# Optimization experiments

Measured on AMD Instinct MI355X. Metric: run time of the kernel, lower is better.

Reference implementation:

```python
import jax, jax.numpy as jnp
import numpy as np
import math

N_NODES = 100000
N_EDGES = 1600000
IN_C, HID_C, OUT_C = 512, 128, 64
N_LAYERS = 8
ALPHA = 0.1
THETA = 0.5


def setup_inputs() -> dict:
    key = jax.random.key(0)
    ks = jax.random.split(key, 6)
    x = jax.random.normal(ks[0], (N_NODES, IN_C), dtype=jnp.float32)
    edge_index = jax.random.randint(ks[1], (2, N_EDGES), 0, N_NODES, dtype=jnp.int32)
    edge_weight = jax.random.uniform(ks[2], (N_EDGES,), dtype=jnp.float32)
    # parameters (scaled for numerical sanity)
    W_enc = jax.random.normal(ks[3], (HID_C, IN_C), dtype=jnp.float32) * (1.0 / math.sqrt(IN_C))
    W_convs = jax.random.normal(ks[4], (N_LAYERS, HID_C, HID_C), dtype=jnp.float32) * (1.0 / math.sqrt(HID_C))
    W_dec = jax.random.normal(ks[5], (OUT_C, HID_C), dtype=jnp.float32) * (1.0 / math.sqrt(HID_C))
    return {"x": x, "edge_index": edge_index, "edge_weight": edge_weight,
            "W_enc": W_enc, "W_convs": W_convs, "W_dec": W_dec}


def reference(x, edge_index, edge_weight, W_enc, W_convs, W_dec):
    # eval mode: dropout is a no-op
    src, dst = edge_index[0], edge_index[1]
    h = x @ W_enc.T                      # [N, HID]
    x0 = h                               # initial residual
    for i in range(N_LAYERS):
        # sparse neighbor aggregation: agg[d] = sum_e w_e * h[src_e]
        msg = h[src] * edge_weight[:, None]                      # [E, HID]
        agg = jax.ops.segment_sum(msg, dst, num_segments=N_NODES)
        hh = (1.0 - ALPHA) * agg + ALPHA * x0                    # initial residual
        beta = math.log(THETA / (i + 1) + 1.0)                   # identity mapping weight
        h = jax.nn.relu((1.0 - beta) * hh + beta * (hh @ W_convs[i]))
    return h @ W_dec.T                   # [N, OUT]
```

## Files before the change

### kernel.cpp

```cpp
#include <hip/hip_runtime.h>
#include <math.h>

#define N_NODES 100000
#define N_EDGES 1600000
#define IN_C 512
#define HID_C 128
#define OUT_C 64
#define N_LAYERS 8

typedef short bf16x8 __attribute__((ext_vector_type(8)));
typedef float f32x4 __attribute__((ext_vector_type(4)));

static __device__ __forceinline__ ushort f2bf(float f) {
  uint u = __float_as_uint(f);
  u = (u + 0x7FFFu + ((u >> 16) & 1u)) >> 16;
  return (ushort)u;
}
static __device__ __forceinline__ float bflo(uint u) { return __uint_as_float(u << 16); }
static __device__ __forceinline__ float bfhi(uint u) { return __uint_as_float(u & 0xffff0000u); }

__global__ __launch_bounds__(256) void hist_kernel(const int* __restrict__ dst,
                                                   int* __restrict__ cnt) {
  int e = blockIdx.x * 256 + threadIdx.x;
  atomicAdd(&cnt[dst[e]], 1);
}

__global__ __launch_bounds__(256) void scan_block(const int* __restrict__ in,
                                                  int* __restrict__ out,
                                                  int* __restrict__ bsum, int n) {
  __shared__ int tsum[256];
  int t = threadIdx.x;
  int base = blockIdx.x * 1024 + t * 4;
  int v0 = (base + 0 < n) ? in[base + 0] : 0;
  int v1 = (base + 1 < n) ? in[base + 1] : 0;
  int v2 = (base + 2 < n) ? in[base + 2] : 0;
  int v3 = (base + 3 < n) ? in[base + 3] : 0;
  int s = v0 + v1 + v2 + v3;
  tsum[t] = s;
  __syncthreads();
  for (int off = 1; off < 256; off <<= 1) {
    int x = (t >= off) ? tsum[t - off] : 0;
    __syncthreads();
    tsum[t] += x;
    __syncthreads();
  }
  int excl = tsum[t] - s;
  int i0 = excl + v0, i1 = i0 + v1, i2 = i1 + v2, i3 = i2 + v3;
  if (base + 0 < n) out[base + 0] = i0;
  if (base + 1 < n) out[base + 1] = i1;
  if (base + 2 < n) out[base + 2] = i2;
  if (base + 3 < n) out[base + 3] = i3;
  if (t == 255 && bsum) bsum[blockIdx.x] = tsum[255];
}

__global__ __launch_bounds__(256) void finalize_rows(const int* __restrict__ incl,
                                                     const int* __restrict__ auxi,
                                                     int* __restrict__ row, int n) {
  int i = blockIdx.x * 256 + threadIdx.x;
  if (i < n) {
    int g = i >> 10;
    int off = g ? auxi[g - 1] : 0;
    row[i + 1] = incl[i] + off;
    if (i == 0) row[0] = 0;
  }
}

__global__ __launch_bounds__(128) void init_bincur(const int* __restrict__ row,
                                                   int* __restrict__ bincur) {
  int b = threadIdx.x;
  int n0 = b << 10;
  bincur[b] = row[n0 < N_NODES ? n0 : N_NODES];
}

__global__ __launch_bounds__(256) void bin_scatter(const int* __restrict__ src,
                                                   const int* __restrict__ dst,
                                                   const float* __restrict__ w,
                                                   int* __restrict__ bincur,
                                                   uint2* __restrict__ bb) {
  __shared__ uint2 ebuf[2048];
  __shared__ int hist[128];
  __shared__ int lstart[128];
  __shared__ int gbase[128];
  int tid = threadIdx.x;
  int base = blockIdx.x * 2048;
  int cnt = N_EDGES - base;
  if (cnt > 2048) cnt = 2048;
  if (tid < 128) hist[tid] = 0;
  __syncthreads();
  uint pay[8];
  int bn[8], rk[8], dfull[8];
#pragma unroll
  for (int i = 0; i < 8; i++) {
    int idx = tid + i * 256;
    if (idx < cnt) {
      int e = base + idx;
      int d = dst[e];
      uint fb = __float_as_uint(w[e]) + 0x8000u;
      pay[i] = ((fb >> 16) << 17) | (uint)src[e];
      dfull[i] = d;
      bn[i] = d >> 10;
      rk[i] = atomicAdd(&hist[bn[i]], 1);
    }
  }
  __syncthreads();
  if (tid == 0) {
    int acc = 0;
    for (int b = 0; b < 128; b++) { lstart[b] = acc; acc += hist[b]; }
  }
  __syncthreads();
  if (tid < 128 && hist[tid] > 0) gbase[tid] = atomicAdd(&bincur[tid], hist[tid]);
  __syncthreads();
#pragma unroll
  for (int i = 0; i < 8; i++) {
    int idx = tid + i * 256;
    if (idx < cnt) ebuf[lstart[bn[i]] + rk[i]] = make_uint2(pay[i], (uint)dfull[i]);
  }
  __syncthreads();
#pragma unroll
  for (int i = 0; i < 8; i++) {
    int j = tid + i * 256;
    if (j < cnt) {
      uint2 v = ebuf[j];
      int b = (int)(v.y >> 10);
      bb[gbase[b] + (j - lstart[b])] = v;
    }
  }
}

__global__ __launch_bounds__(256) void bin_place(const uint2* __restrict__ bb,
                                                 const int* __restrict__ row,
                                                 uint* __restrict__ epk) {
  __shared__ int lcur[1024];
  int b = blockIdx.x;
  int n0 = b << 10;
  int tid = threadIdx.x;
  for (int i = tid; i < 1024; i += 256) {
    int d = n0 + i;
    lcur[i] = (d < N_NODES) ? row[d] : 0;
  }
  __syncthreads();
  int hi = n0 + 1024;
  if (hi > N_NODES) hi = N_NODES;
  int beg = row[n0], end = row[hi];
  for (int j = beg + tid; j < end; j += 256) {
    uint2 v = bb[j];
    int p = atomicAdd(&lcur[v.y & 1023u], 1);
    epk[p] = v.x;
  }
}

__global__ __launch_bounds__(256) void cast_weights(const float* __restrict__ we,
                                                    const float* __restrict__ wc,
                                                    const float* __restrict__ wd,
                                                    ushort* __restrict__ web,
                                                    ushort* __restrict__ wcb,
                                                    ushort* __restrict__ wdb) {
  int i = blockIdx.x * 256 + threadIdx.x;
  if (i < 128 * 512) web[i] = f2bf(we[i]);
  if (i < 8 * 128 * 128) {
    int layer = i >> 14, rem = i & 16383, k = rem >> 7, j = rem & 127;
    wcb[(layer << 14) + (j << 7) + k] = f2bf(wc[i]);
  }
  if (i < 64 * 128) wdb[i] = f2bf(wd[i]);
}

__global__ __launch_bounds__(256) void enc_mfma(const float* __restrict__ x,
                                                const ushort* __restrict__ wb,
                                                ushort* __restrict__ h) {
  __shared__ ushort xs[32][136];
  __shared__ ushort ws[128][136];
  int tid = threadIdx.x;
  size_t row0 = (size_t)blockIdx.x * 32;
  int lane = tid & 63;
  int wv = tid >> 6;
  int m0 = (wv >> 1) * 16;
  int n0 = (wv & 1) * 64;
  int arow = m0 + (lane & 15);
  int akb = (lane >> 4) * 8;
  f32x4 acc[4] = {};
  for (int kc = 0; kc < 4; kc++) {
    int k0 = kc * 128;
    __syncthreads();
#pragma unroll
    for (int i = 0; i < 4; i++) {
      int u = tid + i * 256;
      int r = u >> 5, c4 = u & 31;
      float4 v = *(const float4*)(x + (row0 + r) * IN_C + k0 + c4 * 4);
      uint2 p;
      p.x = (uint)f2bf(v.x) | ((uint)f2bf(v.y) << 16);
      p.y = (uint)f2bf(v.z) | ((uint)f2bf(v.w) << 16);
      *(uint2*)&xs[r][c4 * 4] = p;
    }
#pragma unroll
    for (int i = 0; i < 8; i++) {
      int u = tid + i * 256;
      int c = u >> 4, o = u & 15;
      *(uint4*)&ws[c][o * 8] = *(const uint4*)(wb + (size_t)c * IN_C + k0 + o * 8);
    }
    __syncthreads();
#pragma unroll
    for (int ks = 0; ks < 4; ks++) {
      int kk = ks * 32 + akb;
      bf16x8 a = *(bf16x8*)&xs[arow][kk];
#pragma unroll
      for (int n = 0; n < 4; n++) {
        bf16x8 b = *(bf16x8*)&ws[n0 + n * 16 + (lane & 15)][kk];
        acc[n] = __builtin_amdgcn_mfma_f32_16x16x32_bf16(a, b, acc[n], 0, 0, 0);
      }
    }
  }
  int crow = m0 + (lane >> 4) * 4;
  int ccol = lane & 15;
#pragma unroll
  for (int n = 0; n < 4; n++)
#pragma unroll
    for (int r = 0; r < 4; r++)
      h[(row0 + crow + r) * HID_C + n0 + n * 16 + ccol] = f2bf(acc[n][r]);
}

__global__ __launch_bounds__(256) void agg_bf(const ushort* __restrict__ h,
                                              const ushort* __restrict__ x0,
                                              const int* __restrict__ row,
                                              const uint* __restrict__ epk,
                                              ushort* __restrict__ out) {
  int node = (blockIdx.x * 256 + threadIdx.x) >> 6;
  int lane = threadIdx.x & 63;
  int beg = row[node], end = row[node + 1];
  float a0 = 0.f, a1 = 0.f;
  const uint* hp = (const uint*)h + lane;
  for (int e = beg; e < end; e += 8) {
    uint p0 = (e + 0 < end) ? epk[e + 0] : 0u;
    uint p1 = (e + 1 < end) ? epk[e + 1] : 0u;
    uint p2 = (e + 2 < end) ? epk[e + 2] : 0u;
    uint p3 = (e + 3 < end) ? epk[e + 3] : 0u;
    uint p4 = (e + 4 < end) ? epk[e + 4] : 0u;
    uint p5 = (e + 5 < end) ? epk[e + 5] : 0u;
    uint p6 = (e + 6 < end) ? epk[e + 6] : 0u;
    uint p7 = (e + 7 < end) ? epk[e + 7] : 0u;
    uint h0 = hp[(size_t)(p0 & 0x1FFFFu) * 64];
    uint h1 = hp[(size_t)(p1 & 0x1FFFFu) * 64];
    uint h2 = hp[(size_t)(p2 & 0x1FFFFu) * 64];
    uint h3 = hp[(size_t)(p3 & 0x1FFFFu) * 64];
    uint h4 = hp[(size_t)(p4 & 0x1FFFFu) * 64];
    uint h5 = hp[(size_t)(p5 & 0x1FFFFu) * 64];
    uint h6 = hp[(size_t)(p6 & 0x1FFFFu) * 64];
    uint h7 = hp[(size_t)(p7 & 0x1FFFFu) * 64];
    float w0 = __uint_as_float((p0 >> 17) << 16);
    float w1 = __uint_as_float((p1 >> 17) << 16);
    float w2 = __uint_as_float((p2 >> 17) << 16);
    float w3 = __uint_as_float((p3 >> 17) << 16);
    float w4 = __uint_as_float((p4 >> 17) << 16);
    float w5 = __uint_as_float((p5 >> 17) << 16);
    float w6 = __uint_as_float((p6 >> 17) << 16);
    float w7 = __uint_as_float((p7 >> 17) << 16);
    a0 = fmaf(w0, bflo(h0), a0); a1 = fmaf(w0, bfhi(h0), a1);
    a0 = fmaf(w1, bflo(h1), a0); a1 = fmaf(w1, bfhi(h1), a1);
    a0 = fmaf(w2, bflo(h2), a0); a1 = fmaf(w2, bfhi(h2), a1);
    a0 = fmaf(w3, bflo(h3), a0); a1 = fmaf(w3, bfhi(h3), a1);
    a0 = fmaf(w4, bflo(h4), a0); a1 = fmaf(w4, bfhi(h4), a1);
    a0 = fmaf(w5, bflo(h5), a0); a1 = fmaf(w5, bfhi(h5), a1);
    a0 = fmaf(w6, bflo(h6), a0); a1 = fmaf(w6, bfhi(h6), a1);
    a0 = fmaf(w7, bflo(h7), a0); a1 = fmaf(w7, bfhi(h7), a1);
  }
  uint xv = ((const uint*)x0)[(size_t)node * 64 + lane];
  float o0 = 0.9f * a0 + 0.1f * bflo(xv);
  float o1 = 0.9f * a1 + 0.1f * bfhi(xv);
  ((uint*)out)[(size_t)node * 64 + lane] = (uint)f2bf(o0) | ((uint)f2bf(o1) << 16);
}

__global__ __launch_bounds__(256) void conv_mfma(ushort* __restrict__ hbuf,
                                                 const ushort* __restrict__ wb,
                                                 float onemb, float beta) {
  __shared__ ushort hs[64][136];
  __shared__ ushort ws[128][136];
  int tid = threadIdx.x;
  size_t row0 = (size_t)blockIdx.x * 64;
#pragma unroll
  for (int i = 0; i < 4; i++) {
    int u = tid + i * 256;
    int r = u >> 4, o = u & 15;
    if (row0 + r < N_NODES)
      *(uint4*)&hs[r][o * 8] = *(const uint4*)(hbuf + (row0 + r) * HID_C + o * 8);
  }
#pragma unroll
  for (int i = 0; i < 8; i++) {
    int u = tid + i * 256;
    int c = u >> 4, o = u & 15;
    *(uint4*)&ws[c][o * 8] = *(const uint4*)(wb + (size_t)c * HID_C + o * 8);
  }
  __syncthreads();
  int lane = tid & 63;
  int wv = tid >> 6;
  int m0 = wv * 16;
  int arow = m0 + (lane & 15), akb = (lane >> 4) * 8;
  f32x4 acc[8] = {};
#pragma unroll
  for (int ks = 0; ks < 4; ks++) {
    int kk = ks * 32 + akb;
    bf16x8 a = *(bf16x8*)&hs[arow][kk];
#pragma unroll
    for (int n = 0; n < 8; n++) {
      bf16x8 b = *(bf16x8*)&ws[n * 16 + (lane & 15)][kk];
      acc[n] = __builtin_amdgcn_mfma_f32_16x16x32_bf16(a, b, acc[n], 0, 0, 0);
    }
  }
  int crow = m0 + (lane >> 4) * 4, ccol = lane & 15;
#pragma unroll
  for (int n = 0; n < 8; n++)
#pragma unroll
    for (int r = 0; r < 4; r++) {
      if (row0 + crow + r < N_NODES) {
        float hv = bflo((uint)hs[crow + r][n * 16 + ccol]);
        float o = fmaxf(onemb * hv + beta * acc[n][r], 0.f);
        hbuf[(row0 + crow + r) * HID_C + n * 16 + ccol] = f2bf(o);
      }
    }
}

__global__ __launch_bounds__(256) void dec_mfma(const ushort* __restrict__ h,
                                                const ushort* __restrict__ wb,
                                                float* __restrict__ out) {
  __shared__ ushort hs[32][136];
  __shared__ ushort ws[64][136];
  int tid = threadIdx.x;
  size_t row0 = (size_t)blockIdx.x * 32;
  {
    int r = tid >> 3, o = tid & 7;
    *(uint4*)&hs[r][o * 16] = *(const uint4*)(h + (row0 + r) * HID_C + o * 16);
    *(uint4*)&hs[r][o * 16 + 8] = *(const uint4*)(h + (row0 + r) * HID_C + o * 16 + 8);
  }
#pragma unroll
  for (int i = 0; i < 4; i++) {
    int u = tid + i * 256;
    int c = u >> 4, o = u & 15;
    *(uint4*)&ws[c][o * 8] = *(const uint4*)(wb + (size_t)c * HID_C + o * 8);
  }
  __syncthreads();
  int lane = tid & 63, wv = tid >> 6;
  int m0 = (wv >> 1) * 16, n0 = (wv & 1) * 32;
  int arow = m0 + (lane & 15), akb = (lane >> 4) * 8;
  f32x4 acc[2] = {};
#pragma unroll
  for (int ks = 0; ks < 4; ks++) {
    int kk = ks * 32 + akb;
    bf16x8 a = *(bf16x8*)&hs[arow][kk];
#pragma unroll
    for (int n = 0; n < 2; n++) {
      bf16x8 b = *(bf16x8*)&ws[n0 + n * 16 + (lane & 15)][kk];
      acc[n] = __builtin_amdgcn_mfma_f32_16x16x32_bf16(a, b, acc[n], 0, 0, 0);
    }
  }
  int crow = m0 + (lane >> 4) * 4, ccol = lane & 15;
#pragma unroll
  for (int n = 0; n < 2; n++)
#pragma unroll
    for (int r = 0; r < 4; r++)
      out[(row0 + crow + r) * OUT_C + n0 + n * 16 + ccol] = acc[n][r];
}

extern "C" void kernel_launch(void* const* d_in, const int* in_sizes, int n_in,
                              void* d_out, int out_size, void* d_ws, size_t ws_size,
                              hipStream_t stream) {
  const float* x = (const float*)d_in[0];
  const int* ei = (const int*)d_in[1];
  const float* ew = (const float*)d_in[2];
  const float* Wenc = (const float*)d_in[3];
  const float* Wconvs = (const float*)d_in[4];
  const float* Wdec = (const float*)d_in[5];
  float* out = (float*)d_out;

  char* p = (char*)d_ws;
  ushort* H0 = (ushort*)p; p += (size_t)N_NODES * HID_C * 2;
  ushort* HA = (ushort*)p; p += (size_t)N_NODES * HID_C * 2;
  ushort* HB = (ushort*)p; p += (size_t)N_NODES * HID_C * 2;
  uint* EPK = (uint*)p;    p += (size_t)N_EDGES * 4;
  uint2* BB = (uint2*)p;   p += (size_t)N_EDGES * 8;
  ushort* WENC = (ushort*)p;  p += 128 * 512 * 2;
  ushort* WCONV = (ushort*)p; p += 8 * 128 * 128 * 2;
  ushort* WDEC = (ushort*)p;  p += 64 * 128 * 2;
  int* ROW = (int*)p;  p += (N_NODES + 1) * 4;
  int* CNT = (int*)p;  p += N_NODES * 4;
  int* INCL = (int*)p; p += N_NODES * 4;
  int* BINCUR = (int*)p; p += 128 * 4;
  int* AUX = (int*)p;  p += 128 * 4;
  int* AUXI = (int*)p;

  const int* src = ei;
  const int* dst = ei + N_EDGES;

  cast_weights<<<512, 256, 0, stream>>>(Wenc, Wconvs, Wdec, WENC, WCONV, WDEC);

  hipMemsetAsync(CNT, 0, N_NODES * sizeof(int), stream);
  hist_kernel<<<N_EDGES / 256, 256, 0, stream>>>(dst, CNT);
  scan_block<<<98, 256, 0, stream>>>(CNT, INCL, AUX, N_NODES);
  scan_block<<<1, 256, 0, stream>>>(AUX, AUXI, nullptr, 98);
  finalize_rows<<<391, 256, 0, stream>>>(INCL, AUXI, ROW, N_NODES);
  init_bincur<<<1, 128, 0, stream>>>(ROW, BINCUR);
  bin_scatter<<<(N_EDGES + 2047) / 2048, 256, 0, stream>>>(src, dst, ew, BINCUR, BB);
  bin_place<<<98, 256, 0, stream>>>(BB, ROW, EPK);

  enc_mfma<<<3125, 256, 0, stream>>>(x, WENC, H0);

  const ushort* cur = H0;
  ushort* bufs[2] = {HA, HB};
  for (int i = 0; i < N_LAYERS; i++) {
    ushort* nxt = bufs[i & 1];
    agg_bf<<<25000, 256, 0, stream>>>(cur, H0, ROW, EPK, nxt);
    float beta = logf(0.5f / (float)(i + 1) + 1.0f);
    conv_mfma<<<1563, 256, 0, stream>>>(nxt, WCONV + (size_t)i * HID_C * HID_C,
                                        1.0f - beta, beta);
    cur = nxt;
  }

  dec_mfma<<<3125, 256, 0, stream>>>(cur, WDEC, out);
}
```

Measured before the change: 847.7 us.

## Bin edges into fixed-stride buckets first, enlarge encoder tile, deepen gather unroll

```diff
diff --git a/kernel.cpp b/kernel.cpp
--- a/kernel.cpp
+++ b/kernel.cpp
@@ -7,6 +7,7 @@
 #define HID_C 128
 #define OUT_C 64
 #define N_LAYERS 8
+#define BINSTRIDE 18432
 
 typedef short bf16x8 __attribute__((ext_vector_type(8)));
 typedef float f32x4 __attribute__((ext_vector_type(4)));
@@ -19,10 +20,80 @@
 static __device__ __forceinline__ float bflo(uint u) { return __uint_as_float(u << 16); }
 static __device__ __forceinline__ float bfhi(uint u) { return __uint_as_float(u & 0xffff0000u); }
 
-__global__ __launch_bounds__(256) void hist_kernel(const int* __restrict__ dst,
-                                                   int* __restrict__ cnt) {
-  int e = blockIdx.x * 256 + threadIdx.x;
-  atomicAdd(&cnt[dst[e]], 1);
+__global__ __launch_bounds__(128) void init_bincur(int* __restrict__ bincur) {
+  bincur[threadIdx.x] = threadIdx.x * BINSTRIDE;
+}
+
+__global__ __launch_bounds__(256) void bin_scatter(const int* __restrict__ src,
+                                                   const int* __restrict__ dst,
+                                                   const float* __restrict__ w,
+                                                   int* __restrict__ bincur,
+                                                   uint2* __restrict__ bb) {
+  __shared__ uint2 ebuf[2048];
+  __shared__ int hist[128];
+  __shared__ int lstart[128];
+  __shared__ int gbase[128];
+  int tid = threadIdx.x;
+  int base = blockIdx.x * 2048;
+  int cnt = N_EDGES - base;
+  if (cnt > 2048) cnt = 2048;
+  if (tid < 128) hist[tid] = 0;
+  __syncthreads();
+  uint pay[8];
+  int bn[8], rk[8], dfull[8];
+#pragma unroll
+  for (int i = 0; i < 8; i++) {
+    int idx = tid + i * 256;
+    if (idx < cnt) {
+      int e = base + idx;
+      int d = dst[e];
+      uint fb = __float_as_uint(w[e]) + 0x8000u;
+      pay[i] = ((fb >> 16) << 17) | (uint)src[e];
+      dfull[i] = d;
+      bn[i] = d >> 10;
+      rk[i] = atomicAdd(&hist[bn[i]], 1);
+    }
+  }
+  __syncthreads();
+  if (tid == 0) {
+    int acc = 0;
+    for (int b = 0; b < 128; b++) { lstart[b] = acc; acc += hist[b]; }
+  }
+  __syncthreads();
+  if (tid < 128 && hist[tid] > 0) gbase[tid] = atomicAdd(&bincur[tid], hist[tid]);
+  __syncthreads();
+#pragma unroll
+  for (int i = 0; i < 8; i++) {
+    int idx = tid + i * 256;
+    if (idx < cnt) ebuf[lstart[bn[i]] + rk[i]] = make_uint2(pay[i], (uint)dfull[i]);
+  }
+  __syncthreads();
+#pragma unroll
+  for (int i = 0; i < 8; i++) {
+    int j = tid + i * 256;
+    if (j < cnt) {
+      uint2 v = ebuf[j];
+      int b = (int)(v.y >> 10);
+      bb[gbase[b] + (j - lstart[b])] = v;
+    }
+  }
+}
+
+__global__ __launch_bounds__(256) void bin_count(const uint2* __restrict__ bb,
+                                                 const int* __restrict__ bincur,
+                                                 int* __restrict__ cnt) {
+  __shared__ int lc[1024];
+  int b = blockIdx.x;
+  int tid = threadIdx.x;
+  for (int i = tid; i < 1024; i += 256) lc[i] = 0;
+  __syncthreads();
+  int beg = b * BINSTRIDE, end = bincur[b];
+  for (int j = beg + tid; j < end; j += 256)
+    atomicAdd(&lc[bb[j].y & 1023u], 1);
+  __syncthreads();
+  int n0 = b << 10;
+  for (int i = tid; i < 1024; i += 256)
+    if (n0 + i < N_NODES) cnt[n0 + i] = lc[i];
 }
 
 __global__ __launch_bounds__(256) void scan_block(const int* __restrict__ in,
@@ -65,69 +136,8 @@
   }
 }
 
-__global__ __launch_bounds__(128) void init_bincur(const int* __restrict__ row,
-                                                   int* __restrict__ bincur) {
-  int b = threadIdx.x;
-  int n0 = b << 10;
-  bincur[b] = row[n0 < N_NODES ? n0 : N_NODES];
-}
-
-__global__ __launch_bounds__(256) void bin_scatter(const int* __restrict__ src,
-                                                   const int* __restrict__ dst,
-                                                   const float* __restrict__ w,
-                                                   int* __restrict__ bincur,
-                                                   uint2* __restrict__ bb) {
-  __shared__ uint2 ebuf[2048];
-  __shared__ int hist[128];
-  __shared__ int lstart[128];
-  __shared__ int gbase[128];
-  int tid = threadIdx.x;
-  int base = blockIdx.x * 2048;
-  int cnt = N_EDGES - base;
-  if (cnt > 2048) cnt = 2048;
-  if (tid < 128) hist[tid] = 0;
-  __syncthreads();
-  uint pay[8];
-  int bn[8], rk[8], dfull[8];
-#pragma unroll
-  for (int i = 0; i < 8; i++) {
-    int idx = tid + i * 256;
-    if (idx < cnt) {
-      int e = base + idx;
-      int d = dst[e];
-      uint fb = __float_as_uint(w[e]) + 0x8000u;
-      pay[i] = ((fb >> 16) << 17) | (uint)src[e];
-      dfull[i] = d;
-      bn[i] = d >> 10;
-      rk[i] = atomicAdd(&hist[bn[i]], 1);
-    }
-  }
-  __syncthreads();
-  if (tid == 0) {
-    int acc = 0;
-    for (int b = 0; b < 128; b++) { lstart[b] = acc; acc += hist[b]; }
-  }
-  __syncthreads();
-  if (tid < 128 && hist[tid] > 0) gbase[tid] = atomicAdd(&bincur[tid], hist[tid]);
-  __syncthreads();
-#pragma unroll
-  for (int i = 0; i < 8; i++) {
-    int idx = tid + i * 256;
-    if (idx < cnt) ebuf[lstart[bn[i]] + rk[i]] = make_uint2(pay[i], (uint)dfull[i]);
-  }
-  __syncthreads();
-#pragma unroll
-  for (int i = 0; i < 8; i++) {
-    int j = tid + i * 256;
-    if (j < cnt) {
-      uint2 v = ebuf[j];
-      int b = (int)(v.y >> 10);
-      bb[gbase[b] + (j - lstart[b])] = v;
-    }
-  }
-}
-
 __global__ __launch_bounds__(256) void bin_place(const uint2* __restrict__ bb,
+                                                 const int* __restrict__ bincur,
                                                  const int* __restrict__ row,
                                                  uint* __restrict__ epk) {
   __shared__ int lcur[1024];
@@ -139,9 +149,7 @@
     lcur[i] = (d < N_NODES) ? row[d] : 0;
   }
   __syncthreads();
-  int hi = n0 + 1024;
-  if (hi > N_NODES) hi = N_NODES;
-  int beg = row[n0], end = row[hi];
+  int beg = b * BINSTRIDE, end = bincur[b];
   for (int j = beg + tid; j < end; j += 256) {
     uint2 v = bb[j];
     int p = atomicAdd(&lcur[v.y & 1023u], 1);
@@ -167,28 +175,30 @@
 __global__ __launch_bounds__(256) void enc_mfma(const float* __restrict__ x,
                                                 const ushort* __restrict__ wb,
                                                 ushort* __restrict__ h) {
-  __shared__ ushort xs[32][136];
+  __shared__ ushort xs[64][136];
   __shared__ ushort ws[128][136];
   int tid = threadIdx.x;
-  size_t row0 = (size_t)blockIdx.x * 32;
+  size_t row0 = (size_t)blockIdx.x * 64;
   int lane = tid & 63;
   int wv = tid >> 6;
-  int m0 = (wv >> 1) * 16;
+  int m0 = (wv >> 1) * 32;
   int n0 = (wv & 1) * 64;
   int arow = m0 + (lane & 15);
   int akb = (lane >> 4) * 8;
-  f32x4 acc[4] = {};
+  f32x4 acc[2][4] = {};
   for (int kc = 0; kc < 4; kc++) {
     int k0 = kc * 128;
     __syncthreads();
 #pragma unroll
-    for (int i = 0; i < 4; i++) {
+    for (int i = 0; i < 8; i++) {
       int u = tid + i * 256;
       int r = u >> 5, c4 = u & 31;
-      float4 v = *(const float4*)(x + (row0 + r) * IN_C + k0 + c4 * 4);
-      uint2 p;
-      p.x = (uint)f2bf(v.x) | ((uint)f2bf(v.y) << 16);
-      p.y = (uint)f2bf(v.z) | ((uint)f2bf(v.w) << 16);
+      uint2 p = make_uint2(0u, 0u);
+      if (row0 + r < N_NODES) {
+        float4 v = *(const float4*)(x + (row0 + r) * IN_C + k0 + c4 * 4);
+        p.x = (uint)f2bf(v.x) | ((uint)f2bf(v.y) << 16);
+        p.y = (uint)f2bf(v.z) | ((uint)f2bf(v.w) << 16);
+      }
       *(uint2*)&xs[r][c4 * 4] = p;
     }
 #pragma unroll
@@ -201,21 +211,28 @@
 #pragma unroll
     for (int ks = 0; ks < 4; ks++) {
       int kk = ks * 32 + akb;
-      bf16x8 a = *(bf16x8*)&xs[arow][kk];
+      bf16x8 a0 = *(bf16x8*)&xs[arow][kk];
+      bf16x8 a1 = *(bf16x8*)&xs[arow + 16][kk];
 #pragma unroll
       for (int n = 0; n < 4; n++) {
         bf16x8 b = *(bf16x8*)&ws[n0 + n * 16 + (lane & 15)][kk];
-        acc[n] = __builtin_amdgcn_mfma_f32_16x16x32_bf16(a, b, acc[n], 0, 0, 0);
+        acc[0][n] = __builtin_amdgcn_mfma_f32_16x16x32_bf16(a0, b, acc[0][n], 0, 0, 0);
+        acc[1][n] = __builtin_amdgcn_mfma_f32_16x16x32_bf16(a1, b, acc[1][n], 0, 0, 0);
       }
     }
   }
   int crow = m0 + (lane >> 4) * 4;
   int ccol = lane & 15;
 #pragma unroll
-  for (int n = 0; n < 4; n++)
-#pragma unroll
-    for (int r = 0; r < 4; r++)
-      h[(row0 + crow + r) * HID_C + n0 + n * 16 + ccol] = f2bf(acc[n][r]);
+  for (int m = 0; m < 2; m++)
+#pragma unroll
+    for (int n = 0; n < 4; n++)
+#pragma unroll
+      for (int r = 0; r < 4; r++) {
+        size_t rr = row0 + crow + m * 16 + r;
+        if (rr < N_NODES)
+          h[rr * HID_C + n0 + n * 16 + ccol] = f2bf(acc[m][n][r]);
+      }
 }
 
 __global__ __launch_bounds__(256) void agg_bf(const ushort* __restrict__ h,
@@ -228,39 +245,19 @@
   int beg = row[node], end = row[node + 1];
   float a0 = 0.f, a1 = 0.f;
   const uint* hp = (const uint*)h + lane;
-  for (int e = beg; e < end; e += 8) {
-    uint p0 = (e + 0 < end) ? epk[e + 0] : 0u;
-    uint p1 = (e + 1 < end) ? epk[e + 1] : 0u;
-    uint p2 = (e + 2 < end) ? epk[e + 2] : 0u;
-    uint p3 = (e + 3 < end) ? epk[e + 3] : 0u;
-    uint p4 = (e + 4 < end) ? epk[e + 4] : 0u;
-    uint p5 = (e + 5 < end) ? epk[e + 5] : 0u;
-    uint p6 = (e + 6 < end) ? epk[e + 6] : 0u;
-    uint p7 = (e + 7 < end) ? epk[e + 7] : 0u;
-    uint h0 = hp[(size_t)(p0 & 0x1FFFFu) * 64];
-    uint h1 = hp[(size_t)(p1 & 0x1FFFFu) * 64];
-    uint h2 = hp[(size_t)(p2 & 0x1FFFFu) * 64];
-    uint h3 = hp[(size_t)(p3 & 0x1FFFFu) * 64];
-    uint h4 = hp[(size_t)(p4 & 0x1FFFFu) * 64];
-    uint h5 = hp[(size_t)(p5 & 0x1FFFFu) * 64];
-    uint h6 = hp[(size_t)(p6 & 0x1FFFFu) * 64];
-    uint h7 = hp[(size_t)(p7 & 0x1FFFFu) * 64];
-    float w0 = __uint_as_float((p0 >> 17) << 16);
-    float w1 = __uint_as_float((p1 >> 17) << 16);
-    float w2 = __uint_as_float((p2 >> 17) << 16);
-    float w3 = __uint_as_float((p3 >> 17) << 16);
-    float w4 = __uint_as_float((p4 >> 17) << 16);
-    float w5 = __uint_as_float((p5 >> 17) << 16);
-    float w6 = __uint_as_float((p6 >> 17) << 16);
-    float w7 = __uint_as_float((p7 >> 17) << 16);
-    a0 = fmaf(w0, bflo(h0), a0); a1 = fmaf(w0, bfhi(h0), a1);
-    a0 = fmaf(w1, bflo(h1), a0); a1 = fmaf(w1, bfhi(h1), a1);
-    a0 = fmaf(w2, bflo(h2), a0); a1 = fmaf(w2, bfhi(h2), a1);
-    a0 = fmaf(w3, bflo(h3), a0); a1 = fmaf(w3, bfhi(h3), a1);
-    a0 = fmaf(w4, bflo(h4), a0); a1 = fmaf(w4, bfhi(h4), a1);
-    a0 = fmaf(w5, bflo(h5), a0); a1 = fmaf(w5, bfhi(h5), a1);
-    a0 = fmaf(w6, bflo(h6), a0); a1 = fmaf(w6, bfhi(h6), a1);
-    a0 = fmaf(w7, bflo(h7), a0); a1 = fmaf(w7, bfhi(h7), a1);
+  for (int e = beg; e < end; e += 16) {
+    uint pv[16];
+    uint hv[16];
+#pragma unroll
+    for (int k = 0; k < 16; k++) pv[k] = (e + k < end) ? epk[e + k] : 0u;
+#pragma unroll
+    for (int k = 0; k < 16; k++) hv[k] = hp[(size_t)(pv[k] & 0x1FFFFu) * 64];
+#pragma unroll
+    for (int k = 0; k < 16; k++) {
+      float w = __uint_as_float((pv[k] >> 17) << 16);
+      a0 = fmaf(w, bflo(hv[k]), a0);
+      a1 = fmaf(w, bfhi(hv[k]), a1);
+    }
   }
   uint xv = ((const uint*)x0)[(size_t)node * 64 + lane];
   float o0 = 0.9f * a0 + 0.1f * bflo(xv);
@@ -374,7 +371,7 @@
   ushort* HA = (ushort*)p; p += (size_t)N_NODES * HID_C * 2;
   ushort* HB = (ushort*)p; p += (size_t)N_NODES * HID_C * 2;
   uint* EPK = (uint*)p;    p += (size_t)N_EDGES * 4;
-  uint2* BB = (uint2*)p;   p += (size_t)N_EDGES * 8;
+  uint2* BB = (uint2*)p;   p += (size_t)128 * BINSTRIDE * 8;
   ushort* WENC = (ushort*)p;  p += 128 * 512 * 2;
   ushort* WCONV = (ushort*)p; p += 8 * 128 * 128 * 2;
   ushort* WDEC = (ushort*)p;  p += 64 * 128 * 2;
@@ -390,16 +387,15 @@
 
   cast_weights<<<512, 256, 0, stream>>>(Wenc, Wconvs, Wdec, WENC, WCONV, WDEC);
 
-  hipMemsetAsync(CNT, 0, N_NODES * sizeof(int), stream);
-  hist_kernel<<<N_EDGES / 256, 256, 0, stream>>>(dst, CNT);
+  init_bincur<<<1, 128, 0, stream>>>(BINCUR);
+  bin_scatter<<<(N_EDGES + 2047) / 2048, 256, 0, stream>>>(src, dst, ew, BINCUR, BB);
+  bin_count<<<98, 256, 0, stream>>>(BB, BINCUR, CNT);
   scan_block<<<98, 256, 0, stream>>>(CNT, INCL, AUX, N_NODES);
   scan_block<<<1, 256, 0, stream>>>(AUX, AUXI, nullptr, 98);
   finalize_rows<<<391, 256, 0, stream>>>(INCL, AUXI, ROW, N_NODES);
-  init_bincur<<<1, 128, 0, stream>>>(ROW, BINCUR);
-  bin_scatter<<<(N_EDGES + 2047) / 2048, 256, 0, stream>>>(src, dst, ew, BINCUR, BB);
-  bin_place<<<98, 256, 0, stream>>>(BB, ROW, EPK);
-
-  enc_mfma<<<3125, 256, 0, stream>>>(x, WENC, H0);
+  bin_place<<<98, 256, 0, stream>>>(BB, BINCUR, ROW, EPK);
+
+  enc_mfma<<<1563, 256, 0, stream>>>(x, WENC, H0);
 
   const ushort* cur = H0;
   ushort* bufs[2] = {HA, HB};
```

Result: faster. 820.1 us (-3.3%).
